# Performance work log

Measured on AMD Instinct MI355X. Metric: run time of the kernel, lower is better.

The kernel has to match this reference:

```python
import jax, jax.numpy as jnp
import numpy as np

B, S, D, H = 2, 2048, 1024, 16
HD = D // H  # head_dim = 64


def setup_inputs() -> dict:
    key = jax.random.key(0)
    ks = jax.random.split(key, 12)
    sc = 1.0 / np.sqrt(D)
    return {
        "query": jax.random.normal(ks[0], (B, S, D), jnp.float32),
        "key_": jax.random.normal(ks[1], (B, S, D), jnp.float32),
        "value": jax.random.normal(ks[2], (B, S, D), jnp.float32),
        "mask": jax.random.randint(ks[3], (B, 1, S, S), 0, 2, jnp.int32),
        "Wq": jax.random.normal(ks[4], (D, D), jnp.float32) * sc,
        "bq": jnp.zeros((D,), jnp.float32),
        "Wk": jax.random.normal(ks[5], (D, D), jnp.float32) * sc,
        "bk": jnp.zeros((D,), jnp.float32),
        "Wv": jax.random.normal(ks[6], (D, D), jnp.float32) * sc,
        "bv": jnp.zeros((D,), jnp.float32),
        "Wo": jax.random.normal(ks[7], (D, D), jnp.float32) * sc,
        "bo": jnp.zeros((D,), jnp.float32),
    }


def _split(x):
    # [B, S, D] -> [B, H, S, HD]
    return x.reshape(B, S, H, HD).transpose(0, 2, 1, 3)


def reference(query, key_, value, mask, Wq, bq, Wk, bk, Wv, bv, Wo, bo):
    Q = _split(query @ Wq + bq)
    K = _split(key_ @ Wk + bk)
    V = _split(value @ Wv + bv)
    # scores: [B, H, Sq, Sk]
    scores = jnp.einsum("bhqd,bhkd->bhqk", Q, K) / jnp.sqrt(jnp.float32(HD))
    scores = jnp.where(mask == 0, jnp.float32(-1e9), scores)
    probs = jax.nn.softmax(scores, axis=-1)
    attn = jnp.einsum("bhqk,bhkd->bhqd", probs, V)
    out = attn.transpose(0, 2, 1, 3).reshape(B, S, D)
    return out @ Wo + bo
```

## Files before the change

kernel.cpp:

```cpp
#include <hip/hip_runtime.h>
#include <stdint.h>

typedef _Float16 f16;
typedef _Float16 f16x2 __attribute__((ext_vector_type(2)));
typedef _Float16 f16x4 __attribute__((ext_vector_type(4)));
typedef _Float16 f16x8 __attribute__((ext_vector_type(8)));
typedef __fp16 hf16x2 __attribute__((ext_vector_type(2)));
typedef float f32x4 __attribute__((ext_vector_type(4)));
typedef float f32x16 __attribute__((ext_vector_type(16)));
typedef unsigned u32;
typedef unsigned uint2v __attribute__((ext_vector_type(2)));

static constexpr int Bb = 2, Ss = 2048, Dd = 1024, Hh = 16, HDd = 64;
static constexpr int M_ROWS = Bb * Ss;

static constexpr size_t OFF_X   = 0;
static constexpr size_t OFF_WT  = 24ull << 20;
static constexpr size_t OFF_QKV = 32ull << 20;
static constexpr size_t OFF_ATT = 56ull << 20;
static constexpr size_t OFF_MB  = 64ull << 20;

__device__ __forceinline__ void gll16(const void* g, void* l) {
  __builtin_amdgcn_global_load_lds((__attribute__((address_space(1))) const void*)g,
                                   (__attribute__((address_space(3))) void*)l, 16, 0, 0);
}

__device__ __forceinline__ int lds_byte(int row, int slot) {
  return row * 128 + (((slot ^ (row & 7)) & 7) << 4);
}

__device__ __forceinline__ float ex2(float x) {
  float r; asm("v_exp_f32 %0, %1" : "=v"(r) : "v"(x)); return r;
}

union H2U { hf16x2 h; u32 u; };

__global__ __launch_bounds__(256) void cvt_x(const float* __restrict__ q,
                                             const float* __restrict__ k,
                                             const float* __restrict__ v,
                                             f16* __restrict__ out) {
  const float* src = blockIdx.z == 0 ? q : blockIdx.z == 1 ? k : v;
  f16* dst = out + (size_t)blockIdx.z * M_ROWS * Dd;
  int i = blockIdx.x * 256 + threadIdx.x;
  float4 a = reinterpret_cast<const float4*>(src)[i];
  f16x4 o;
  o[0] = (f16)a.x; o[1] = (f16)a.y; o[2] = (f16)a.z; o[3] = (f16)a.w;
  *reinterpret_cast<f16x4*>(dst + (size_t)i * 4) = o;
}

__global__ __launch_bounds__(256) void cvt_wt(const float* __restrict__ wq,
                                              const float* __restrict__ wk,
                                              const float* __restrict__ wv,
                                              const float* __restrict__ wo,
                                              f16* __restrict__ out) {
  const int z = blockIdx.z;
  const float* W = z == 0 ? wq : z == 1 ? wk : z == 2 ? wv : wo;
  f16* Wt = out + (size_t)z * Dd * Dd;
  __shared__ float t[32][33];
  const int tx = threadIdx.x, ty = threadIdx.y;
  const int k0 = blockIdx.y * 32, n0 = blockIdx.x * 32;
  for (int i = 0; i < 32; i += 8) t[ty + i][tx] = W[(size_t)(k0 + ty + i) * Dd + n0 + tx];
  __syncthreads();
  for (int i = 0; i < 32; i += 8) Wt[(size_t)(n0 + ty + i) * Dd + k0 + tx] = (f16)t[tx][ty + i];
}

__global__ __launch_bounds__(256) void pack_mask(const int* __restrict__ mask,
                                                 unsigned* __restrict__ bits) {
  size_t i = (size_t)blockIdx.x * 256 + threadIdx.x;
  int v = mask[i];
  unsigned long long b = __ballot(v != 0);
  if ((threadIdx.x & 63) == 0) {
    size_t w = i >> 5;
    bits[w]     = (unsigned)b;
    bits[w + 1] = (unsigned)(b >> 32);
  }
}

template<bool F32OUT>
__global__ __launch_bounds__(256) void gemm_bt(const f16* __restrict__ Abase,
                                               const f16* __restrict__ Btbase,
                                               const float* __restrict__ b0,
                                               const float* __restrict__ b1,
                                               const float* __restrict__ b2,
                                               void* __restrict__ Cbase) {
  constexpr int K = Dd, N = Dd;
  const int z = blockIdx.z;
  const f16* A  = Abase  + (size_t)z * M_ROWS * K;
  const f16* Bt = Btbase + (size_t)z * N * K;
  const float* bias = z == 0 ? b0 : z == 1 ? b1 : b2;
  const int m0 = blockIdx.y * 128, n0 = blockIdx.x * 128;
  __shared__ f16 As[128 * 64], Bs[128 * 64];
  const int tid = threadIdx.x, l = tid & 63, w = tid >> 6;
  const int li = l & 15, g = l >> 4;
  const int wm = (w >> 1) * 64, wn = (w & 1) * 64;
  const int sr = l >> 3, ss = l & 7;

  f32x4 acc[4][4];
  for (int mi = 0; mi < 4; mi++)
    for (int ni = 0; ni < 4; ni++) acc[mi][ni] = f32x4{0.f, 0.f, 0.f, 0.f};

  for (int kt = 0; kt < K; kt += 64) {
    __syncthreads();
    for (int c = 0; c < 4; c++) {
      int chunk = w * 4 + c;
      int r = chunk * 8 + sr;
      int col = ((ss ^ (r & 7)) << 3);
      gll16(A  + (size_t)(m0 + r) * K + kt + col, (char*)As + chunk * 1024);
      gll16(Bt + (size_t)(n0 + r) * K + kt + col, (char*)Bs + chunk * 1024);
    }
    __syncthreads();
#pragma unroll
    for (int ks = 0; ks < 2; ks++) {
      f16x8 af[4], bf[4];
#pragma unroll
      for (int i = 0; i < 4; i++) {
        af[i] = *(const f16x8*)((const char*)As + lds_byte(wm + i * 16 + li, ks * 4 + g));
        bf[i] = *(const f16x8*)((const char*)Bs + lds_byte(wn + i * 16 + li, ks * 4 + g));
      }
#pragma unroll
      for (int mi = 0; mi < 4; mi++)
#pragma unroll
        for (int ni = 0; ni < 4; ni++)
          acc[mi][ni] = __builtin_amdgcn_mfma_f32_16x16x32_f16(af[mi], bf[ni], acc[mi][ni], 0, 0, 0);
    }
  }
  const float scl = (!F32OUT && z == 0) ? 0.18033688011112042f : 1.0f;
  if (!F32OUT && z == 2) {
    f16* Vt = (f16*)Cbase + (size_t)z * M_ROWS * N;
#pragma unroll
    for (int mi = 0; mi < 4; mi++)
#pragma unroll
      for (int ni = 0; ni < 4; ni++) {
        const int col = n0 + wn + ni * 16 + li;
        const int r0  = m0 + wm + mi * 16 + g * 4;
        const int bb_ = r0 >> 11, s = r0 & 2047;
        const float bv = bias[col];
        f16x4 pk;
#pragma unroll
        for (int j = 0; j < 4; j++) pk[j] = (f16)(acc[mi][ni][j] + bv);
        *(f16x4*)(Vt + ((size_t)(bb_ * Hh) << 17) + (size_t)col * Ss + s) = pk;
      }
  } else {
    for (int mi = 0; mi < 4; mi++)
      for (int ni = 0; ni < 4; ni++) {
        const int r0  = m0 + wm + mi * 16 + g * 4;
        const int col = n0 + wn + ni * 16 + li;
        const float bb = bias[col];
#pragma unroll
        for (int j = 0; j < 4; j++) {
          float val = (acc[mi][ni][j] + bb) * scl;
          if (F32OUT) ((float*)Cbase)[(size_t)(r0 + j) * N + col] = val;
          else ((f16*)Cbase)[(size_t)z * M_ROWS * N + (size_t)(r0 + j) * N + col] = (f16)val;
        }
      }
  }
}

__global__ __launch_bounds__(512, 4) void attn_fused(const f16* __restrict__ Qp,
                                                     const f16* __restrict__ Kp,
                                                     const f16* __restrict__ Vt,
                                                     const u32* __restrict__ mbits,
                                                     f16* __restrict__ outp) {
  const int flat = blockIdx.x;
  const int xcd = flat & 7, jj = flat >> 3;
  const int qt = jj & 15;
  const int hb = xcd * 4 + (jj >> 4);
  const int h = hb & 15, b = hb >> 4;

  const int tid = threadIdx.x, l = tid & 63, w = tid >> 6;
  const int lo = l & 31, hi = l >> 5;
  const int half = w >> 2, wsub = w & 3;
  const int q0 = qt * 128, wq = wsub * 32;

  __shared__ char smem[65536];
  char* hbase = smem + half * 32768;
  char* Qst = smem + 16384;

  const size_t qkbase = (size_t)b * Ss * Dd + (size_t)h * HDd;
  const f16* Vtb = Vt + (size_t)(b * Hh + h) * HDd * Ss;
  const int sr = l >> 3, ss = l & 7;
  const int scol = ((ss ^ sr) << 3);

  for (int c = 0; c < 2; c++) {
    int chunk = w * 2 + c, r = chunk * 8 + sr;
    gll16(Qp + qkbase + (size_t)(q0 + r) * Dd + scol, Qst + chunk * 1024);
  }
  const int kt0 = half * 16;
  for (int c = 0; c < 2; c++) {
    int chunk = wsub * 2 + c, r = chunk * 8 + sr;
    gll16(Kp + qkbase + (size_t)(kt0 * 64 + r) * Dd + scol, hbase + chunk * 1024);
    gll16(Vtb + (size_t)r * Ss + kt0 * 64 + scol, hbase + 8192 + chunk * 1024);
  }
  __syncthreads();

  f16x8 qf[4];
#pragma unroll
  for (int c = 0; c < 4; c++)
    qf[c] = *(const f16x8*)(Qst + lds_byte(wq + lo, 2 * c + hi));
  __syncthreads();

  f32x16 accO0 = {0}, accO1 = {0};
  float m_run = -1e30f, l_run = 0.f;
  const u32* mrow = mbits + (size_t)(b * Ss + q0 + wq + lo) * 64;

  for (int it = 0; it < 16; it++) {
    const int kt = kt0 + it;
    if (it) __syncthreads();
    char* bufc = hbase + (it & 1) * 16384;
    if (it < 15) {
      char* bufn = hbase + ((it + 1) & 1) * 16384;
      const int k0n = (kt + 1) * 64;
      for (int c = 0; c < 2; c++) {
        int chunk = wsub * 2 + c, r = chunk * 8 + sr;
        gll16(Kp + qkbase + (size_t)(k0n + r) * Dd + scol, bufn + chunk * 1024);
        gll16(Vtb + (size_t)r * Ss + k0n + scol, bufn + 8192 + chunk * 1024);
      }
    }
    const char* Kb = bufc;
    const char* Vb = bufc + 8192;

    f32x16 s0 = {0}, s1 = {0};
    __builtin_amdgcn_s_setprio(1);
#pragma unroll
    for (int c = 0; c < 4; c++) {
      f16x8 kf0 = *(const f16x8*)(Kb + lds_byte(lo, 2 * c + hi));
      f16x8 kf1 = *(const f16x8*)(Kb + lds_byte(32 + lo, 2 * c + hi));
      s0 = __builtin_amdgcn_mfma_f32_32x32x16_f16(kf0, qf[c], s0, 0, 0, 0);
      s1 = __builtin_amdgcn_mfma_f32_32x32x16_f16(kf1, qf[c], s1, 0, 0, 0);
    }
    __builtin_amdgcn_s_setprio(0);

    uint2v mw = *(const uint2v*)(mrow + kt * 2);
    u32 wa = mw.x >> (hi << 2);
    u32 wb = mw.y >> (hi << 2);

    float x0 = fmaxf(s0[0], s1[0]), x1 = fmaxf(s0[1], s1[1]);
    float x2 = fmaxf(s0[2], s1[2]), x3 = fmaxf(s0[3], s1[3]);
#pragma unroll
    for (int r = 4; r < 16; r += 4) {
      x0 = fmaxf(x0, fmaxf(s0[r],     s1[r]));
      x1 = fmaxf(x1, fmaxf(s0[r + 1], s1[r + 1]));
      x2 = fmaxf(x2, fmaxf(s0[r + 2], s1[r + 2]));
      x3 = fmaxf(x3, fmaxf(s0[r + 3], s1[r + 3]));
    }
    float pm = fmaxf(fmaxf(x0, x1), fmaxf(x2, x3));

    float mn;
    if (__all(pm <= m_run + 11.5f)) {
      mn = m_run;
    } else {
      pm = fmaxf(pm, __shfl_xor(pm, 32));
      mn = fmaxf(m_run, pm);
      const float so = ex2(m_run - mn);
      m_run = mn;
      l_run *= so;
      accO0 *= so; accO1 *= so;
    }

    float racc = 0.f;
#pragma unroll
    for (int r = 0; r < 16; r++) {
      const int kk = (r & 3) + 8 * (r >> 2);
      u32 ma = (u32)(((int)(wa << (31 - kk))) >> 31);
      u32 mb = (u32)(((int)(wb << (31 - kk))) >> 31);
      float e0 = __uint_as_float(__float_as_uint(ex2(s0[r] - mn)) & ma);
      float e1 = __uint_as_float(__float_as_uint(ex2(s1[r] - mn)) & mb);
      s0[r] = e0; s1[r] = e1;
      racc += e0 + e1;
    }
    l_run += racc;

    u32 pw[16];
#pragma unroll
    for (int j = 0; j < 8; j++) {
      H2U a, c;
      a.h = __builtin_amdgcn_cvt_pkrtz(s0[2 * j], s0[2 * j + 1]);
      c.h = __builtin_amdgcn_cvt_pkrtz(s1[2 * j], s1[2 * j + 1]);
      pw[j] = a.u; pw[8 + j] = c.u;
    }
#pragma unroll
    for (int c = 0; c < 4; c++) {
      asm volatile("v_permlane32_swap_b32 %0, %1" : "+v"(pw[4 * c]), "+v"(pw[4 * c + 2]));
      asm volatile("v_permlane32_swap_b32 %0, %1" : "+v"(pw[4 * c + 1]), "+v"(pw[4 * c + 3]));
    }

    __builtin_amdgcn_s_setprio(1);
#pragma unroll
    for (int c = 0; c < 4; c++) {
      union { u32 u[4]; f16x8 v; } pu;
      pu.u[0] = pw[4 * c]; pu.u[1] = pw[4 * c + 1];
      pu.u[2] = pw[4 * c + 2]; pu.u[3] = pw[4 * c + 3];
      f16x8 vf0 = *(const f16x8*)(Vb + lds_byte(lo, 2 * c + hi));
      f16x8 vf1 = *(const f16x8*)(Vb + lds_byte(32 + lo, 2 * c + hi));
      accO0 = __builtin_amdgcn_mfma_f32_32x32x16_f16(vf0, pu.v, accO0, 0, 0, 0);
      accO1 = __builtin_amdgcn_mfma_f32_32x32x16_f16(vf1, pu.v, accO1, 0, 0, 0);
    }
    __builtin_amdgcn_s_setprio(0);
  }

  __syncthreads();
  float* mg = (float*)smem;
  if (half == 1) {
    float* p = mg + (size_t)(wsub * 64 + l) * 34;
#pragma unroll
    for (int r = 0; r < 16; r++) { p[r] = accO0[r]; p[16 + r] = accO1[r]; }
    p[32] = m_run; p[33] = l_run;
  }
  __syncthreads();
  if (half == 1) return;

  const float* p = mg + (size_t)(wsub * 64 + l) * 34;
  const float mB = p[32], lB = p[33];
  const float m = fmaxf(m_run, mB);
  const float fA = ex2(m_run - m), fB = ex2(mB - m);
  float lmerged = l_run * fA + lB * fB;
#pragma unroll
  for (int r = 0; r < 16; r++) {
    accO0[r] = accO0[r] * fA + p[r] * fB;
    accO1[r] = accO1[r] * fA + p[16 + r] * fB;
  }
  const float lf = lmerged + __shfl_xor(lmerged, 32);
  const float inv = 1.0f / lf;

  char* Ot = smem + 40960 + wsub * 4096;
#pragma unroll
  for (int j = 0; j < 8; j++) {
    H2U pk;
    pk.h = __builtin_amdgcn_cvt_pkrtz(accO0[2 * j] * inv, accO0[2 * j + 1] * inv);
    int slot = (j >> 1);
    int addr = lo * 128 + (((slot ^ (lo & 7)) & 7) << 4) + 4 * (j & 1) + 8 * hi;
    *(u32*)(Ot + addr) = pk.u;
  }
#pragma unroll
  for (int j = 0; j < 8; j++) {
    H2U pk;
    pk.h = __builtin_amdgcn_cvt_pkrtz(accO1[2 * j] * inv, accO1[2 * j + 1] * inv);
    int slot = (j >> 1) + 4;
    int addr = lo * 128 + (((slot ^ (lo & 7)) & 7) << 4) + 4 * (j & 1) + 8 * hi;
    *(u32*)(Ot + addr) = pk.u;
  }
  asm volatile("s_waitcnt lgkmcnt(0)" ::: "memory");
  {
    const int q = l >> 1, halfq = l & 1;
    f16* gbase = outp + qkbase + (size_t)(q0 + wq + q) * Dd + halfq * 32;
#pragma unroll
    for (int c = 0; c < 4; c++) {
      int byte = q * 128 + ((((halfq * 4 + c) ^ (q & 7)) & 7) << 4);
      f16x8 v = *(const f16x8*)(Ot + byte);
      *(f16x8*)(gbase + c * 8) = v;
    }
  }
}

extern "C" void kernel_launch(void* const* d_in, const int* in_sizes, int n_in,
                              void* d_out, int out_size, void* d_ws, size_t ws_size,
                              hipStream_t stream) {
  const float* query = (const float*)d_in[0];
  const float* key_  = (const float*)d_in[1];
  const float* value = (const float*)d_in[2];
  const int*   mask  = (const int*)d_in[3];
  const float* Wq = (const float*)d_in[4];
  const float* bq = (const float*)d_in[5];
  const float* Wk = (const float*)d_in[6];
  const float* bk = (const float*)d_in[7];
  const float* Wv = (const float*)d_in[8];
  const float* bv = (const float*)d_in[9];
  const float* Wo = (const float*)d_in[10];
  const float* bo = (const float*)d_in[11];

  char* ws = (char*)d_ws;
  f16* X   = (f16*)(ws + OFF_X);
  f16* Wt  = (f16*)(ws + OFF_WT);
  f16* QKV = (f16*)(ws + OFF_QKV);
  f16* ATT = (f16*)(ws + OFF_ATT);
  unsigned* MB = (unsigned*)(ws + OFF_MB);

  cvt_x<<<dim3(4096, 1, 3), 256, 0, stream>>>(query, key_, value, X);
  cvt_wt<<<dim3(32, 32, 4), dim3(32, 8), 0, stream>>>(Wq, Wk, Wv, Wo, Wt);
  pack_mask<<<dim3(32768), 256, 0, stream>>>(mask, MB);
  gemm_bt<false><<<dim3(8, 32, 3), 256, 0, stream>>>(X, Wt, bq, bk, bv, QKV);
  attn_fused<<<dim3(512), 512, 0, stream>>>(QKV, QKV + (size_t)M_ROWS * Dd,
                                            QKV + 2 * (size_t)M_ROWS * Dd, MB, ATT);
  gemm_bt<true><<<dim3(8, 32, 1), 256, 0, stream>>>(ATT, Wt + 3 * (size_t)Dd * Dd,
                                                    bo, bo, bo, d_out);
}
```

Baseline: 161.1 us.

## Fuse fp32-to-fp16 input conversion into QKV GEMM and merge prep kernels

Removes the separate cvt_x kernel: the QKV GEMM now loads fp32 activations directly into registers, converts them to fp16 and writes them to LDS, with a register prefetch of the next K tile. Mask packing and weight transposition are merged into one prep launch. Both GEMMs remap block indices so neighbouring tiles land on the same XCD, and the attention merge scratch stride is padded from 34 to 35 floats to reduce LDS bank conflicts. This saves a full fp16 activation round trip and two launches. The cost is a register-staged A path in place of the async global_load_lds path, which raises register pressure.

```diff
diff --git a/kernel.cpp b/kernel.cpp
--- a/kernel.cpp
+++ b/kernel.cpp
@@ -2,7 +2,6 @@
 #include <stdint.h>
 
 typedef _Float16 f16;
-typedef _Float16 f16x2 __attribute__((ext_vector_type(2)));
 typedef _Float16 f16x4 __attribute__((ext_vector_type(4)));
 typedef _Float16 f16x8 __attribute__((ext_vector_type(8)));
 typedef __fp16 hf16x2 __attribute__((ext_vector_type(2)));
@@ -14,7 +13,6 @@
 static constexpr int Bb = 2, Ss = 2048, Dd = 1024, Hh = 16, HDd = 64;
 static constexpr int M_ROWS = Bb * Ss;
 
-static constexpr size_t OFF_X   = 0;
 static constexpr size_t OFF_WT  = 24ull << 20;
 static constexpr size_t OFF_QKV = 32ull << 20;
 static constexpr size_t OFF_ATT = 56ull << 20;
@@ -35,87 +33,104 @@
 
 union H2U { hf16x2 h; u32 u; };
 
-__global__ __launch_bounds__(256) void cvt_x(const float* __restrict__ q,
-                                             const float* __restrict__ k,
-                                             const float* __restrict__ v,
-                                             f16* __restrict__ out) {
-  const float* src = blockIdx.z == 0 ? q : blockIdx.z == 1 ? k : v;
-  f16* dst = out + (size_t)blockIdx.z * M_ROWS * Dd;
-  int i = blockIdx.x * 256 + threadIdx.x;
-  float4 a = reinterpret_cast<const float4*>(src)[i];
-  f16x4 o;
-  o[0] = (f16)a.x; o[1] = (f16)a.y; o[2] = (f16)a.z; o[3] = (f16)a.w;
-  *reinterpret_cast<f16x4*>(dst + (size_t)i * 4) = o;
-}
-
-__global__ __launch_bounds__(256) void cvt_wt(const float* __restrict__ wq,
-                                              const float* __restrict__ wk,
-                                              const float* __restrict__ wv,
-                                              const float* __restrict__ wo,
-                                              f16* __restrict__ out) {
-  const int z = blockIdx.z;
-  const float* W = z == 0 ? wq : z == 1 ? wk : z == 2 ? wv : wo;
-  f16* Wt = out + (size_t)z * Dd * Dd;
+__global__ __launch_bounds__(256) void prep(const int* __restrict__ mask,
+                                            unsigned* __restrict__ bits,
+                                            const float* __restrict__ wq,
+                                            const float* __restrict__ wk,
+                                            const float* __restrict__ wv,
+                                            const float* __restrict__ wo,
+                                            f16* __restrict__ wt) {
+  const int bid = blockIdx.x;
   __shared__ float t[32][33];
-  const int tx = threadIdx.x, ty = threadIdx.y;
-  const int k0 = blockIdx.y * 32, n0 = blockIdx.x * 32;
-  for (int i = 0; i < 32; i += 8) t[ty + i][tx] = W[(size_t)(k0 + ty + i) * Dd + n0 + tx];
-  __syncthreads();
-  for (int i = 0; i < 32; i += 8) Wt[(size_t)(n0 + ty + i) * Dd + k0 + tx] = (f16)t[tx][ty + i];
-}
-
-__global__ __launch_bounds__(256) void pack_mask(const int* __restrict__ mask,
-                                                 unsigned* __restrict__ bits) {
-  size_t i = (size_t)blockIdx.x * 256 + threadIdx.x;
-  int v = mask[i];
-  unsigned long long b = __ballot(v != 0);
-  if ((threadIdx.x & 63) == 0) {
-    size_t w = i >> 5;
-    bits[w]     = (unsigned)b;
-    bits[w + 1] = (unsigned)(b >> 32);
-  }
-}
-
-template<bool F32OUT>
-__global__ __launch_bounds__(256) void gemm_bt(const f16* __restrict__ Abase,
-                                               const f16* __restrict__ Btbase,
-                                               const float* __restrict__ b0,
-                                               const float* __restrict__ b1,
-                                               const float* __restrict__ b2,
-                                               void* __restrict__ Cbase) {
+  if (bid < 32768) {
+    size_t i = (size_t)bid * 256 + threadIdx.x;
+    int v = mask[i];
+    unsigned long long bm = __ballot(v != 0);
+    if ((threadIdx.x & 63) == 0) {
+      size_t w = i >> 5;
+      bits[w]     = (unsigned)bm;
+      bits[w + 1] = (unsigned)(bm >> 32);
+    }
+  } else {
+    const int wb = bid - 32768;
+    const int z = wb >> 10, by = (wb >> 5) & 31, bx = wb & 31;
+    const float* W = z == 0 ? wq : z == 1 ? wk : z == 2 ? wv : wo;
+    f16* Wt = wt + (size_t)z * Dd * Dd;
+    const int tx = threadIdx.x & 31, ty = threadIdx.x >> 5;
+    const int k0 = by * 32, n0 = bx * 32;
+    for (int i = 0; i < 32; i += 8) t[ty + i][tx] = W[(size_t)(k0 + ty + i) * Dd + n0 + tx];
+    __syncthreads();
+    for (int i = 0; i < 32; i += 8) Wt[(size_t)(n0 + ty + i) * Dd + k0 + tx] = (f16)t[tx][ty + i];
+  }
+}
+
+__global__ __launch_bounds__(256) void gemm_qkv(const float* __restrict__ qin,
+                                                const float* __restrict__ kin,
+                                                const float* __restrict__ vin,
+                                                const f16* __restrict__ Btbase,
+                                                const float* __restrict__ b0,
+                                                const float* __restrict__ b1,
+                                                const float* __restrict__ b2,
+                                                f16* __restrict__ Cbase) {
   constexpr int K = Dd, N = Dd;
-  const int z = blockIdx.z;
-  const f16* A  = Abase  + (size_t)z * M_ROWS * K;
+  const int f = blockIdx.x;
+  const int z = f >> 8, i = f & 255;
+  const int xg = i & 7, sl = i >> 3;
+  const int m0 = (xg * 4 + (sl >> 3)) * 128, n0 = (sl & 7) * 128;
+  const float* A = z == 0 ? qin : z == 1 ? kin : vin;
   const f16* Bt = Btbase + (size_t)z * N * K;
   const float* bias = z == 0 ? b0 : z == 1 ? b1 : b2;
-  const int m0 = blockIdx.y * 128, n0 = blockIdx.x * 128;
   __shared__ f16 As[128 * 64], Bs[128 * 64];
   const int tid = threadIdx.x, l = tid & 63, w = tid >> 6;
-  const int li = l & 15, g = l >> 4;
+  const int li = l & 15, gq = l >> 4;
   const int wm = (w >> 1) * 64, wn = (w & 1) * 64;
   const int sr = l >> 3, ss = l & 7;
+  const int scol = ((ss ^ sr) << 3);
 
   f32x4 acc[4][4];
   for (int mi = 0; mi < 4; mi++)
     for (int ni = 0; ni < 4; ni++) acc[mi][ni] = f32x4{0.f, 0.f, 0.f, 0.f};
 
+  float4 a0[4], a1[4];
+#pragma unroll
+  for (int c = 0; c < 4; c++) {
+    int r = (w * 4 + c) * 8 + sr;
+    const float* src = A + (size_t)(m0 + r) * K + scol;
+    a0[c] = *(const float4*)src; a1[c] = *(const float4*)(src + 4);
+  }
+
   for (int kt = 0; kt < K; kt += 64) {
+    if (kt) __syncthreads();
+#pragma unroll
+    for (int c = 0; c < 4; c++) {
+      const int chunk = w * 4 + c;
+      H2U h0, h1, h2, h3;
+      h0.h = __builtin_amdgcn_cvt_pkrtz(a0[c].x, a0[c].y);
+      h1.h = __builtin_amdgcn_cvt_pkrtz(a0[c].z, a0[c].w);
+      h2.h = __builtin_amdgcn_cvt_pkrtz(a1[c].x, a1[c].y);
+      h3.h = __builtin_amdgcn_cvt_pkrtz(a1[c].z, a1[c].w);
+      union { u32 uu[4]; f16x8 v8; } pk;
+      pk.uu[0] = h0.u; pk.uu[1] = h1.u; pk.uu[2] = h2.u; pk.uu[3] = h3.u;
+      *(f16x8*)((char*)As + chunk * 1024 + l * 16) = pk.v8;
+      int r = chunk * 8 + sr;
+      gll16(Bt + (size_t)(n0 + r) * K + kt + scol, (char*)Bs + chunk * 1024);
+    }
     __syncthreads();
-    for (int c = 0; c < 4; c++) {
-      int chunk = w * 4 + c;
-      int r = chunk * 8 + sr;
-      int col = ((ss ^ (r & 7)) << 3);
-      gll16(A  + (size_t)(m0 + r) * K + kt + col, (char*)As + chunk * 1024);
-      gll16(Bt + (size_t)(n0 + r) * K + kt + col, (char*)Bs + chunk * 1024);
-    }
-    __syncthreads();
+    if (kt + 64 < K) {
+#pragma unroll
+      for (int c = 0; c < 4; c++) {
+        int r = (w * 4 + c) * 8 + sr;
+        const float* src = A + (size_t)(m0 + r) * K + (kt + 64) + scol;
+        a0[c] = *(const float4*)src; a1[c] = *(const float4*)(src + 4);
+      }
+    }
 #pragma unroll
     for (int ks = 0; ks < 2; ks++) {
       f16x8 af[4], bf[4];
 #pragma unroll
-      for (int i = 0; i < 4; i++) {
-        af[i] = *(const f16x8*)((const char*)As + lds_byte(wm + i * 16 + li, ks * 4 + g));
-        bf[i] = *(const f16x8*)((const char*)Bs + lds_byte(wn + i * 16 + li, ks * 4 + g));
+      for (int ii = 0; ii < 4; ii++) {
+        af[ii] = *(const f16x8*)((const char*)As + lds_byte(wm + ii * 16 + li, ks * 4 + gq));
+        bf[ii] = *(const f16x8*)((const char*)Bs + lds_byte(wn + ii * 16 + li, ks * 4 + gq));
       }
 #pragma unroll
       for (int mi = 0; mi < 4; mi++)
@@ -124,15 +139,16 @@
           acc[mi][ni] = __builtin_amdgcn_mfma_f32_16x16x32_f16(af[mi], bf[ni], acc[mi][ni], 0, 0, 0);
     }
   }
-  const float scl = (!F32OUT && z == 0) ? 0.18033688011112042f : 1.0f;
-  if (!F32OUT && z == 2) {
-    f16* Vt = (f16*)Cbase + (size_t)z * M_ROWS * N;
+
+  const float scl = (z == 0) ? 0.18033688011112042f : 1.0f;
+  if (z == 2) {
+    f16* Vt = Cbase + (size_t)2 * M_ROWS * N;
 #pragma unroll
     for (int mi = 0; mi < 4; mi++)
 #pragma unroll
       for (int ni = 0; ni < 4; ni++) {
         const int col = n0 + wn + ni * 16 + li;
-        const int r0  = m0 + wm + mi * 16 + g * 4;
+        const int r0  = m0 + wm + mi * 16 + gq * 4;
         const int bb_ = r0 >> 11, s = r0 & 2047;
         const float bv = bias[col];
         f16x4 pk;
@@ -143,17 +159,70 @@
   } else {
     for (int mi = 0; mi < 4; mi++)
       for (int ni = 0; ni < 4; ni++) {
-        const int r0  = m0 + wm + mi * 16 + g * 4;
+        const int r0  = m0 + wm + mi * 16 + gq * 4;
         const int col = n0 + wn + ni * 16 + li;
         const float bb = bias[col];
 #pragma unroll
         for (int j = 0; j < 4; j++) {
           float val = (acc[mi][ni][j] + bb) * scl;
-          if (F32OUT) ((float*)Cbase)[(size_t)(r0 + j) * N + col] = val;
-          else ((f16*)Cbase)[(size_t)z * M_ROWS * N + (size_t)(r0 + j) * N + col] = (f16)val;
+          Cbase[(size_t)z * M_ROWS * N + (size_t)(r0 + j) * N + col] = (f16)val;
         }
       }
   }
+}
+
+__global__ __launch_bounds__(256) void gemm_out(const f16* __restrict__ A,
+                                                const f16* __restrict__ Bt,
+                                                const float* __restrict__ bias,
+                                                float* __restrict__ C) {
+  constexpr int K = Dd, N = Dd;
+  const int f = blockIdx.x;
+  const int xg = f & 7, sl = f >> 3;
+  const int m0 = (xg * 4 + (sl >> 3)) * 128, n0 = (sl & 7) * 128;
+  __shared__ f16 As[128 * 64], Bs[128 * 64];
+  const int tid = threadIdx.x, l = tid & 63, w = tid >> 6;
+  const int li = l & 15, gq = l >> 4;
+  const int wm = (w >> 1) * 64, wn = (w & 1) * 64;
+  const int sr = l >> 3, ss = l & 7;
+  const int scol = ((ss ^ sr) << 3);
+
+  f32x4 acc[4][4];
+  for (int mi = 0; mi < 4; mi++)
+    for (int ni = 0; ni < 4; ni++) acc[mi][ni] = f32x4{0.f, 0.f, 0.f, 0.f};
+
+  for (int kt = 0; kt < K; kt += 64) {
+    __syncthreads();
+    for (int c = 0; c < 4; c++) {
+      int chunk = w * 4 + c;
+      int r = chunk * 8 + sr;
+      gll16(A  + (size_t)(m0 + r) * K + kt + scol, (char*)As + chunk * 1024);
+      gll16(Bt + (size_t)(n0 + r) * K + kt + scol, (char*)Bs + chunk * 1024);
+    }
+    __syncthreads();
+#pragma unroll
+    for (int ks = 0; ks < 2; ks++) {
+      f16x8 af[4], bf[4];
+#pragma unroll
+      for (int ii = 0; ii < 4; ii++) {
+        af[ii] = *(const f16x8*)((const char*)As + lds_byte(wm + ii * 16 + li, ks * 4 + gq));
+        bf[ii] = *(const f16x8*)((const char*)Bs + lds_byte(wn + ii * 16 + li, ks * 4 + gq));
+      }
+#pragma unroll
+      for (int mi = 0; mi < 4; mi++)
+#pragma unroll
+        for (int ni = 0; ni < 4; ni++)
+          acc[mi][ni] = __builtin_amdgcn_mfma_f32_16x16x32_f16(af[mi], bf[ni], acc[mi][ni], 0, 0, 0);
+    }
+  }
+  for (int mi = 0; mi < 4; mi++)
+    for (int ni = 0; ni < 4; ni++) {
+      const int r0  = m0 + wm + mi * 16 + gq * 4;
+      const int col = n0 + wn + ni * 16 + li;
+      const float bb = bias[col];
+#pragma unroll
+      for (int j = 0; j < 4; j++)
+        C[(size_t)(r0 + j) * N + col] = acc[mi][ni][j] + bb;
+    }
 }
 
 __global__ __launch_bounds__(512, 4) void attn_fused(const f16* __restrict__ Qp,
@@ -301,7 +370,7 @@
   __syncthreads();
   float* mg = (float*)smem;
   if (half == 1) {
-    float* p = mg + (size_t)(wsub * 64 + l) * 34;
+    float* p = mg + (size_t)(wsub * 64 + l) * 35;
 #pragma unroll
     for (int r = 0; r < 16; r++) { p[r] = accO0[r]; p[16 + r] = accO1[r]; }
     p[32] = m_run; p[33] = l_run;
@@ -309,7 +378,7 @@
   __syncthreads();
   if (half == 1) return;
 
-  const float* p = mg + (size_t)(wsub * 64 + l) * 34;
+  const float* p = mg + (size_t)(wsub * 64 + l) * 35;
   const float mB = p[32], lB = p[33];
   const float m = fmaxf(m_run, mB);
   const float fA = ex2(m_run - m), fB = ex2(mB - m);
@@ -369,18 +438,14 @@
   const float* bo = (const float*)d_in[11];
 
   char* ws = (char*)d_ws;
-  f16* X   = (f16*)(ws + OFF_X);
   f16* Wt  = (f16*)(ws + OFF_WT);
   f16* QKV = (f16*)(ws + OFF_QKV);
   f16* ATT = (f16*)(ws + OFF_ATT);
   unsigned* MB = (unsigned*)(ws + OFF_MB);
 
-  cvt_x<<<dim3(4096, 1, 3), 256, 0, stream>>>(query, key_, value, X);
-  cvt_wt<<<dim3(32, 32, 4), dim3(32, 8), 0, stream>>>(Wq, Wk, Wv, Wo, Wt);
-  pack_mask<<<dim3(32768), 256, 0, stream>>>(mask, MB);
-  gemm_bt<false><<<dim3(8, 32, 3), 256, 0, stream>>>(X, Wt, bq, bk, bv, QKV);
+  prep<<<dim3(32768 + 4096), 256, 0, stream>>>(mask, MB, Wq, Wk, Wv, Wo, Wt);
+  gemm_qkv<<<dim3(768), 256, 0, stream>>>(query, key_, value, Wt, bq, bk, bv, QKV);
   attn_fused<<<dim3(512), 512, 0, stream>>>(QKV, QKV + (size_t)M_ROWS * Dd,
                                             QKV + 2 * (size_t)M_ROWS * Dd, MB, ATT);
-  gemm_bt<true><<<dim3(8, 32, 1), 256, 0, stream>>>(ATT, Wt + 3 * (size_t)Dd * Dd,
-                                                    bo, bo, bo, d_out);
-}
+  gemm_out<<<dim3(256), 256, 0, stream>>>(ATT, Wt + 3 * (size_t)Dd * Dd, bo, (float*)d_out);
+}
```

Measured after the change: 146.0 us. -9.4%, faster.
